# Kernel tuning notes

Measured on AMD Instinct MI355X. Metric: run time of the kernel, lower is better.

The kernel has to match this reference:

```python
import jax, jax.numpy as jnp
import numpy as np


def lstm(x, W, U, b):
    """Keras LSTM with activation='relu', recurrent_activation='sigmoid'.
    x: [B, S, E]; W: [E, 4u]; U: [u, 4u]; b: [4u]. Gate order i,f,c,o.
    Returns (all hidden states [B,S,u], last hidden [B,u])."""
    B = x.shape[0]
    u = U.shape[0]
    h0 = jnp.zeros((B, u), x.dtype)
    c0 = jnp.zeros((B, u), x.dtype)

    def step(carry, xt):
        h, c = carry
        z = xt @ W + h @ U + b
        i, f, g, o = jnp.split(z, 4, axis=-1)
        i = jax.nn.sigmoid(i)
        f = jax.nn.sigmoid(f)
        g = jax.nn.relu(g)          # candidate activation = relu
        o = jax.nn.sigmoid(o)
        c = f * c + i * g
        h = o * jax.nn.relu(c)      # output activation = relu
        return (h, c), h

    (hT, _), hs = jax.lax.scan(step, (h0, c0), jnp.swapaxes(x, 0, 1))
    return jnp.swapaxes(hs, 0, 1), hT


def setup_inputs() -> dict:
    key = jax.random.key(0)
    ks = iter(jax.random.split(key, 64))

    def W(*s):
        return jax.random.normal(next(ks), s, jnp.float32) * 0.05

    V = 32000
    inp = {
        "t": jax.random.randint(next(ks), (8, 16, 64), 0, V, jnp.int32),
        "p": jax.random.randint(next(ks), (8, 16, 512), 0, V, jnp.int32),
        "emb_t": W(V, 128),
        "emb_p": W(V, 256),
        # title LSTMs: 128 (return_seq) -> 64
        "tl0_W": W(128, 512), "tl0_U": W(128, 512), "tl0_b": jnp.zeros((512,), jnp.float32),
        "tl1_W": W(128, 256), "tl1_U": W(64, 256),  "tl1_b": jnp.zeros((256,), jnp.float32),
        # title dense: 128 relu, 64 relu, 32 linear
        "td0_W": W(64, 128),  "td0_b": jnp.zeros((128,), jnp.float32),
        "td1_W": W(128, 64),  "td1_b": jnp.zeros((64,), jnp.float32),
        "td2_W": W(64, 32),   "td2_b": jnp.zeros((32,), jnp.float32),
        # parag LSTMs: 256 (rs) -> 128 (rs) -> 64
        "pl0_W": W(256, 1024), "pl0_U": W(256, 1024), "pl0_b": jnp.zeros((1024,), jnp.float32),
        "pl1_W": W(256, 512),  "pl1_U": W(128, 512),  "pl1_b": jnp.zeros((512,), jnp.float32),
        "pl2_W": W(128, 256),  "pl2_U": W(64, 256),   "pl2_b": jnp.zeros((256,), jnp.float32),
        # parag dense: 128 relu, 64 relu, 32 linear
        "pd0_W": W(64, 128),  "pd0_b": jnp.zeros((128,), jnp.float32),
        "pd1_W": W(128, 64),  "pd1_b": jnp.zeros((64,), jnp.float32),
        "pd2_W": W(64, 32),   "pd2_b": jnp.zeros((32,), jnp.float32),
        # head: 256 relu, 128 relu, 64 relu, 32 sigmoid
        "L0_W": W(64, 256),  "L0_b": jnp.zeros((256,), jnp.float32),
        "L1_W": W(256, 128), "L1_b": jnp.zeros((128,), jnp.float32),
        "L2_W": W(128, 64),  "L2_b": jnp.zeros((64,), jnp.float32),
        "L3_W": W(64, 32),   "L3_b": jnp.zeros((32,), jnp.float32),
    }
    return inp


def reference(t, p, emb_t, emb_p,
              tl0_W, tl0_U, tl0_b, tl1_W, tl1_U, tl1_b,
              td0_W, td0_b, td1_W, td1_b, td2_W, td2_b,
              pl0_W, pl0_U, pl0_b, pl1_W, pl1_U, pl1_b, pl2_W, pl2_U, pl2_b,
              pd0_W, pd0_b, pd1_W, pd1_b, pd2_W, pd2_b,
              L0_W, L0_b, L1_W, L1_b, L2_W, L2_b, L3_W, L3_b):
    B, N, St = t.shape
    Sp = p.shape[2]

    # The original loops over B and map_fn over a singleton axis; the math is
    # identical to running the stacks on a flattened [B*N] recurrent batch.
    xt = emb_t[t.reshape(B * N, St)]              # [BN, St, 128]
    xt, _ = lstm(xt, tl0_W, tl0_U, tl0_b)         # [BN, St, 128]
    _, ht = lstm(xt, tl1_W, tl1_U, tl1_b)         # [BN, 64]
    ht = jax.nn.relu(ht @ td0_W + td0_b)
    ht = jax.nn.relu(ht @ td1_W + td1_b)
    ht = ht @ td2_W + td2_b                       # [BN, 32] (no activation)

    xp = emb_p[p.reshape(B * N, Sp)]              # [BN, Sp, 256]
    xp, _ = lstm(xp, pl0_W, pl0_U, pl0_b)
    xp, _ = lstm(xp, pl1_W, pl1_U, pl1_b)
    _, hp = lstm(xp, pl2_W, pl2_U, pl2_b)         # [BN, 64]
    hp = jax.nn.relu(hp @ pd0_W + pd0_b)
    hp = jax.nn.relu(hp @ pd1_W + pd1_b)
    hp = hp @ pd2_W + pd2_b                       # [BN, 32]

    feat = jnp.concatenate([ht, hp], axis=-1).reshape(B, N, 64)
    x = feat.mean(axis=1)                         # reduce_mean over axis=-2 (N)
    x = jax.nn.relu(x @ L0_W + L0_b)
    x = jax.nn.relu(x @ L1_W + L1_b)
    x = jax.nn.relu(x @ L2_W + L2_b)
    x = jax.nn.sigmoid(x @ L3_W + L3_b)           # [B, 32]
    return x
```

## Files before the change

kernel.cpp:

```cpp
#include <hip/hip_runtime.h>
#include <hip/hip_fp16.h>

typedef _Float16 f16;
typedef _Float16 f16x8 __attribute__((ext_vector_type(8)));
typedef float    f32x4 __attribute__((ext_vector_type(4)));
typedef unsigned short ushort;
typedef unsigned int uint;
typedef unsigned long long u64;

__device__ __forceinline__ float sigm(float x) { return 1.f / (1.f + __expf(-x)); }
__device__ __forceinline__ float reluf(float x) { return x > 0.f ? x : 0.f; }
__device__ __forceinline__ float h2f(ushort u) { return (float)__builtin_bit_cast(f16, u); }
__device__ __forceinline__ ushort f2h(float v) { return __builtin_bit_cast(ushort, (f16)v); }

#define LDRLX(p)    __hip_atomic_load((p), __ATOMIC_RELAXED, __HIP_MEMORY_SCOPE_AGENT)
#define STRLX(p, v) __hip_atomic_store((p), (v), __ATOMIC_RELAXED, __HIP_MEMORY_SCOPE_AGENT)
#define MFMA16(a, b, c) __builtin_amdgcn_mfma_f32_16x16x32_f16((a), (b), (c), 0, 0, 0)

__device__ __forceinline__ void poll_all(uint* p, uint need, bool act) {
  bool done = !act;
  while (true) {
    if (!done) done = (LDRLX(p) >= need);
    if (__all((int)done)) break;
    __builtin_amdgcn_s_sleep(1);
  }
}

__device__ __forceinline__ u64 ldr64(const u64* p) {
  return __hip_atomic_load(p, __ATOMIC_RELAXED, __HIP_MEMORY_SCOPE_AGENT);
}
__device__ __forceinline__ void str64(u64* p, u64 v) {
  __hip_atomic_store(p, v, __ATOMIC_RELAXED, __HIP_MEMORY_SCOPE_AGENT);
}

template <int NR>
__device__ __forceinline__ void poll_recs(const u64* const (&ra)[NR],
                                          const uint (&nd)[NR], u64 (&rv)[NR]) {
  bool ok[NR];
#pragma unroll
  for (int i = 0; i < NR; i++) ok[i] = (nd[i] == 0u);
  while (true) {
    bool all = true;
#pragma unroll
    for (int i = 0; i < NR; i++) if (!ok[i]) rv[i] = ldr64(ra[i]);
#pragma unroll
    for (int i = 0; i < NR; i++) if (!ok[i]) ok[i] = ((uint)(rv[i] >> 32) >= nd[i]);
#pragma unroll
    for (int i = 0; i < NR; i++) all &= ok[i];
    if (all) return;
    __builtin_amdgcn_s_sleep(1);
  }
}

template <int KF>
__global__ void pack_bsw(const float* __restrict__ B, f16* __restrict__ dst, int N) {
  int id = blockIdx.x * 256 + threadIdx.x;
  int total = KF * 32 * N;
  if (id >= total) return;
  int j  = id & 7;
  int L  = (id >> 3) & 63;
  int r  = id >> 9;
  int kf = r & (KF - 1);
  int c  = r / KF;
  int k  = kf * 32 + ((L >> 4) * 8) + j;
  int n  = c * 16 + (L & 15);
  dst[id] = (f16)B[k * N + n];
}

template <int Sx, int K, int KF, int N, int NC, int MODE>
__global__ __launch_bounds__(256) void gemm_xw(const int* __restrict__ tok,
                                               const float* __restrict__ emb,
                                               const f16* __restrict__ Bsw,
                                               const float* __restrict__ bias,
                                               f16* __restrict__ X) {
  __shared__ int tokLds[64];
  __shared__ f16x8 bLds[8 * 64];
  const int tid = threadIdx.x;
  const int blk = blockIdx.x;
  const int g  = (MODE == 0) ? (blk >> 7) : (blk >> 4);
  const int t0 = (MODE == 0) ? ((blk & 127) * 4) : ((blk & 15) * 4);
  if (tid < 64) {
    int wv = tid >> 4, rho = tid & 15;
    tokLds[tid] = tok[(g * 16 + rho) * Sx + t0 + wv];
  }
  __syncthreads();
  const int wave = tid >> 6, lane = tid & 63;
  const int quad = lane >> 4, l16 = lane & 15;

  f16x8 a[KF];
  {
    const float* arow = emb + (long)tokLds[wave * 16 + l16] * K + quad * 8;
#pragma unroll
    for (int kf = 0; kf < KF; kf++) {
      float4 v0 = *(const float4*)(arow + kf * 32);
      float4 v1 = *(const float4*)(arow + kf * 32 + 4);
      f16x8 tv;
      tv[0] = (f16)v0.x; tv[1] = (f16)v0.y; tv[2] = (f16)v0.z; tv[3] = (f16)v0.w;
      tv[4] = (f16)v1.x; tv[5] = (f16)v1.y; tv[6] = (f16)v1.z; tv[7] = (f16)v1.w;
      a[kf] = tv;
    }
  }
  const int t = t0 + wave;
  const f16x8* Bfrag = (const f16x8*)Bsw;
  for (int c = 0; c < NC; c++) {
    for (int i = tid; i < KF * 64; i += 256) bLds[i] = Bfrag[c * KF * 64 + i];
    __syncthreads();
    f32x4 acc = {0.f, 0.f, 0.f, 0.f};
#pragma unroll
    for (int kf = 0; kf < KF; kf++)
      acc = MFMA16(a[kf], bLds[kf * 64 + lane], acc);
    const int col = c * 16 + l16;
    const float bc = bias[col];
    uint2 pk;
    pk.x = (uint)f2h(acc[0] + bc) | ((uint)f2h(acc[1] + bc) << 16);
    pk.y = (uint)f2h(acc[2] + bc) | ((uint)f2h(acc[3] + bc) << 16);
    size_t base;
    if (MODE == 0) {
      int gm = col >> 8, u = col & 255;
      base = (((size_t)(g * 512 + t) * 4 + gm) * 4096) + u * 16 + quad * 4;
    } else {
      int gm = col >> 7, u = col & 127;
      base = (((size_t)(g * 64 + t) * 4 + gm) * 2048) + u * 16 + quad * 4;
    }
    *(uint2*)(X + base) = pk;
    __syncthreads();
  }
}

struct RP {
  const f16 *xp2, *xt2;
  const f16 *U0f, *W1f, *U1f, *W2f, *U2f, *U0tf, *W1tf, *U1tf;
  const float *pl1_b, *pl2_b, *tl1_b;
  const float *pd0W, *pd0b, *pd1W, *pd1b, *pd2W, *pd2b;
  const float *td0W, *td0b, *td1W, *td1b, *td2W, *td2b;
  u64 *h0r, *h1r, *h0tr;
  uint *cnt;
  float* feat;
};

__global__ __launch_bounds__(256, 1) void recur_pipe(RP A) {
  __shared__ __align__(16) char smem[147968];
  const int tid = threadIdx.x;
  const int w = tid >> 6, lane = tid & 63;
  const int quad = lane >> 4, l16 = lane & 15;
  const int blk = blockIdx.x;
  const int role = blk >> 3, g = blk & 7;
  uint* mytag = A.cnt + (role * 8 + g) * 16;

  if (role < 4) {
    const int bb = role;
    f16* wlds = (f16*)smem;
    f16* hb   = (f16*)(smem + 131072);
    {
      const uint4* U0q = (const uint4*)A.U0f;
      uint4* wq = (uint4*)wlds;
      for (int idx = tid; idx < 8192; idx += 256) {
        int gm = idx >> 11, r = idx & 2047, wv = r >> 9, kf = (r >> 6) & 7, ln = r & 63;
        wq[idx] = U0q[((gm * 16 + 4 * bb + wv) * 8 + kf) * 64 + ln];
      }
    }
    for (int idx = tid; idx < 4224; idx += 256) hb[idx] = (f16)0.f;
    float c0[4] = {0.f, 0.f, 0.f, 0.f};
    u64* ringg = A.h0r + (size_t)g * 16384;
    int pp[3]; { int q = 0; for (int p = 0; p < 4; p++) if (p != bb) pp[q++] = p; }
    const uint2* xq2 = (const uint2*)A.xp2;
    const f16x8* wv8 = (const f16x8*)wlds;
    const int myu = 64 * bb + 16 * w + l16;
    uint* bpp = A.cnt;
    if (lane < 4) bpp = A.cnt + ((4 + lane) * 8 + g) * 16;
    __syncthreads();

    for (int t = 0; t < 512; t++) {
      uint2 xv[4];
      {
        size_t xb = ((size_t)(g * 512 + t) * 4) * 1024 + (size_t)myu * 4 + quad;
#pragma unroll
        for (int gm = 0; gm < 4; gm++) xv[gm] = xq2[xb + (size_t)gm * 1024];
      }
      {
        bool act = (lane < 4) && (t > 0) && ((t & 3) == 0);
        uint need = t > 4 ? (uint)(t - 4) : 0u;
        poll_all(bpp, need, act);
      }
      {
        const u64* slotb = ringg + (size_t)((t + 7) & 7) * 2048;
        const u64* ra[6]; uint nd[6]; u64 rv[6];
#pragma unroll
        for (int q = 0; q < 3; q++) {
          const u64* rb = slotb + pp[q] * 512 + 2 * tid;
          ra[q * 2] = rb; ra[q * 2 + 1] = rb + 1;
          nd[q * 2] = nd[q * 2 + 1] = (t > 0) ? (uint)t : 0u;
        }
        poll_recs<6>(ra, nd, rv);
        if (t > 0) {
          f16* dst = hb + (t & 1) * 4224;
          const int ul = tid >> 2;
#pragma unroll
          for (int q = 0; q < 3; q++)
#pragma unroll
            for (int j = 0; j < 2; j++) {
              uint pay = (uint)rv[q * 2 + j];
              int r0 = ((tid & 3) * 2 + j) * 2;
              dst[r0 * 264 + pp[q] * 64 + ul] = __builtin_bit_cast(f16, (ushort)pay);
              dst[(r0 + 1) * 264 + pp[q] * 64 + ul] = __builtin_bit_cast(f16, (ushort)(pay >> 16));
            }
        }
      }
      __syncthreads();
      f16x8 af[8];
#pragma unroll
      for (int kf = 0; kf < 8; kf++)
        af[kf] = *(const f16x8*)&hb[(t & 1) * 4224 + l16 * 264 + kf * 32 + quad * 8];
      f32x4 z[4];
#pragma unroll
      for (int gm = 0; gm < 4; gm++) {
        f32x4 zz = {0.f, 0.f, 0.f, 0.f};
#pragma unroll
        for (int kf = 0; kf < 8; kf++)
          zz = MFMA16(af[kf], wv8[((gm * 4 + w) * 8 + kf) * 64 + lane], zz);
        z[gm] = zz;
      }
      u64 xs[4];
#pragma unroll
      for (int gm = 0; gm < 4; gm++) xs[gm] = ((u64)xv[gm].y << 32) | xv[gm].x;
      ushort hs[4];
      f16* wbuf = hb + ((t + 1) & 1) * 4224;
#pragma unroll
      for (int r = 0; r < 4; r++) {
        float gi = sigm(z[0][r] + h2f((ushort)(xs[0] >> (16 * r))));
        float ff = sigm(z[1][r] + h2f((ushort)(xs[1] >> (16 * r))));
        float gg = reluf(z[2][r] + h2f((ushort)(xs[2] >> (16 * r))));
        float oo = sigm(z[3][r] + h2f((ushort)(xs[3] >> (16 * r))));
        c0[r] = ff * c0[r] + gi * gg;
        hs[r] = f2h(oo * reluf(c0[r]));
        wbuf[(quad * 4 + r) * 264 + myu] = __builtin_bit_cast(f16, hs[r]);
      }
      {
        u64 tg = ((u64)(uint)(t + 1)) << 32;
        u64* wb = ringg + (size_t)(t & 7) * 2048 + bb * 512 + (16 * w + l16) * 8 + quad * 2;
        str64(wb,     tg | (u64)((uint)hs[0] | ((uint)hs[1] << 16)));
        str64(wb + 1, tg | (u64)((uint)hs[2] | ((uint)hs[3] << 16)));
      }
    }
  } else if (role < 8) {
    const int bn = role - 4;
    f16* wlds = (f16*)smem;
    f16* h0c  = (f16*)(smem + 98304);
    f16* h1b  = (f16*)(smem + 106752);
    float* zL = (float*)(smem + 115456);
    {
      const uint4* W1q = (const uint4*)A.W1f;
      const uint4* U1q = (const uint4*)A.U1f;
      uint4* wq = (uint4*)wlds;
      for (int idx = tid; idx < 4096; idx += 256) {
        int gm = idx >> 10, r = idx & 1023, j2 = r >> 9, kf = (r >> 6) & 7, ln = r & 63;
        wq[idx] = W1q[((gm * 8 + bn * 2 + j2) * 8 + kf) * 64 + ln];
      }
      for (int idx = tid; idx < 2048; idx += 256) {
        int gm = idx >> 9, r = idx & 511, j2 = r >> 8, kf = (r >> 6) & 3, ln = r & 63;
        wq[4096 + idx] = U1q[((gm * 8 + bn * 2 + j2) * 4 + kf) * 64 + ln];
      }
    }
    for (int idx = tid; idx < 2176; idx += 256) h1b[idx] = (f16)0.f;
    float c1[2] = {0.f, 0.f};
    float bth[4];
    { int un = tid & 31; for (int gm = 0; gm < 4; gm++) bth[gm] = A.pl1_b[gm * 128 + 32 * bn + un]; }
    u64* h0rg = A.h0r + (size_t)g * 16384;
    u64* h1rg = A.h1r + (size_t)g * 8192;
    int pp[3]; { int q = 0; for (int p = 0; p < 4; p++) if (p != bn) pp[q++] = p; }
    const f16x8* wv8 = (const f16x8*)wlds;
    uint* bpp = A.cnt + (8 * 8 + g) * 16;
    __syncthreads();

    for (int t = 0; t < 512; t++) {
      {
        bool act = (lane == 0) && ((t & 3) == 0);
        uint need = t > 4 ? (uint)(t - 4) : 0u;
        poll_all(bpp, need, act);
      }
      const u64* ra[11]; uint nd[11]; u64 rv[11];
      {
        const u64* s0b = h0rg + (size_t)(t & 7) * 2048;
#pragma unroll
        for (int e = 0; e < 8; e++) { ra[e] = s0b + tid + 256 * e; nd[e] = (uint)(t + 1); }
        const u64* s1b = h1rg + (size_t)((t + 7) & 7) * 1024;
#pragma unroll
        for (int q = 0; q < 3; q++) { ra[8 + q] = s1b + pp[q] * 256 + tid; nd[8 + q] = (t > 0) ? (uint)t : 0u; }
      }
      poll_recs<11>(ra, nd, rv);
      {
#pragma unroll
        for (int e = 0; e < 8; e++) {
          int idx = tid + 256 * e;
          int q = idx >> 9, rr = idx & 511, uls = rr >> 3, rp = rr & 7;
          uint pay = (uint)rv[e];
          h0c[(2 * rp) * 264 + q * 64 + uls]     = __builtin_bit_cast(f16, (ushort)pay);
          h0c[(2 * rp + 1) * 264 + q * 64 + uls] = __builtin_bit_cast(f16, (ushort)(pay >> 16));
        }
        if (t > 0) {
          f16* dst = h1b + (t & 1) * 2176;
          int un = tid >> 3, sq = tid & 7;
#pragma unroll
          for (int q = 0; q < 3; q++) {
            uint pay = (uint)rv[8 + q];
            dst[sq * 136 + pp[q] * 32 + un]       = __builtin_bit_cast(f16, (ushort)pay);
            dst[(sq + 8) * 136 + pp[q] * 32 + un] = __builtin_bit_cast(f16, (ushort)(pay >> 16));
          }
        }
      }
      __syncthreads();
      if (tid == 0) STRLX(mytag, (uint)(t + 1));
      f16x8 af0[8], af1[4];
#pragma unroll
      for (int kf = 0; kf < 8; kf++)
        af0[kf] = *(const f16x8*)&h0c[l16 * 264 + kf * 32 + quad * 8];
#pragma unroll
      for (int kf = 0; kf < 4; kf++)
        af1[kf] = *(const f16x8*)&h1b[(t & 1) * 2176 + l16 * 136 + kf * 32 + quad * 8];
#pragma unroll
      for (int j2 = 0; j2 < 2; j2++) {
        f32x4 zz = {0.f, 0.f, 0.f, 0.f};
#pragma unroll
        for (int kf = 0; kf < 8; kf++)
          zz = MFMA16(af0[kf], wv8[((w * 2 + j2) * 8 + kf) * 64 + lane], zz);
#pragma unroll
        for (int kf = 0; kf < 4; kf++)
          zz = MFMA16(af1[kf], wv8[4096 + ((w * 2 + j2) * 4 + kf) * 64 + lane], zz);
#pragma unroll
        for (int r = 0; r < 4; r++)
          zL[(quad * 4 + r) * 132 + w * 32 + j2 * 16 + l16] = zz[r];
      }
      __syncthreads();
      {
        int sq = tid >> 5, un = tid & 31;
        f16* dst = h1b + ((t + 1) & 1) * 2176;
        ushort hh[2];
#pragma unroll
        for (int e = 0; e < 2; e++) {
          int s = sq + 8 * e;
          float gi = sigm(zL[s * 132 + un] + bth[0]);
          float ff = sigm(zL[s * 132 + 32 + un] + bth[1]);
          float gg = reluf(zL[s * 132 + 64 + un] + bth[2]);
          float oo = sigm(zL[s * 132 + 96 + un] + bth[3]);
          c1[e] = ff * c1[e] + gi * gg;
          float hv = oo * reluf(c1[e]);
          hh[e] = f2h(hv);
          dst[s * 136 + 32 * bn + un] = __builtin_bit_cast(f16, hh[e]);
        }
        u64 tg = ((u64)(uint)(t + 1)) << 32;
        str64(h1rg + (size_t)(t & 7) * 1024 + bn * 256 + un * 8 + sq,
              tg | (u64)((uint)hh[0] | ((uint)hh[1] << 16)));
      }
    }
  } else if (role == 8) {
    f16* wlds = (f16*)smem;
    f16* h1c  = (f16*)(smem + 98304);
    f16* h2db = (f16*)(smem + 107008);
    {
      const uint4* W2q = (const uint4*)A.W2f;
      const uint4* U2q = (const uint4*)A.U2f;
      uint4* wq = (uint4*)wlds;
      for (int idx = tid; idx < 4096; idx += 256) wq[idx] = W2q[idx];
      for (int idx = tid; idx < 2048; idx += 256) wq[4096 + idx] = U2q[idx];
    }
    for (int idx = tid; idx < 1152; idx += 256) h2db[idx] = (f16)0.f;
    float c2[4] = {0.f, 0.f, 0.f, 0.f};
    float b2[4];
#pragma unroll
    for (int gm = 0; gm < 4; gm++) b2[gm] = A.pl2_b[gm * 64 + 16 * w + l16];
    u64* h1rg = A.h1r + (size_t)g * 8192;
    const f16x8* wv8 = (const f16x8*)wlds;
    __syncthreads();

    for (int t = 0; t < 512; t++) {
      const u64* ra[4]; uint nd[4]; u64 rv[4];
      {
        const u64* s1b = h1rg + (size_t)(t & 7) * 1024;
#pragma unroll
        for (int e = 0; e < 4; e++) { ra[e] = s1b + tid + 256 * e; nd[e] = (uint)(t + 1); }
      }
      poll_recs<4>(ra, nd, rv);
      {
        f16* dst = h1c + (t & 1) * 2176;
#pragma unroll
        for (int e = 0; e < 4; e++) {
          int idx = tid + 256 * e;
          int bq = idx >> 8, rr = idx & 255, un = rr >> 3, sq = rr & 7;
          uint pay = (uint)rv[e];
          dst[sq * 136 + bq * 32 + un]       = __builtin_bit_cast(f16, (ushort)pay);
          dst[(sq + 8) * 136 + bq * 32 + un] = __builtin_bit_cast(f16, (ushort)(pay >> 16));
        }
      }
      __syncthreads();
      if (tid == 0) STRLX(mytag, (uint)(t + 1));
      f16x8 af0[4], af1[2];
#pragma unroll
      for (int kf = 0; kf < 4; kf++)
        af0[kf] = *(const f16x8*)&h1c[(t & 1) * 2176 + l16 * 136 + kf * 32 + quad * 8];
#pragma unroll
      for (int kf = 0; kf < 2; kf++)
        af1[kf] = *(const f16x8*)&h2db[(t & 1) * 1152 + l16 * 72 + kf * 32 + quad * 8];
      f32x4 z[4];
#pragma unroll
      for (int gm = 0; gm < 4; gm++) {
        f32x4 zz = {0.f, 0.f, 0.f, 0.f};
#pragma unroll
        for (int kf = 0; kf < 4; kf++)
          zz = MFMA16(af0[kf], wv8[((gm * 4 + w) * 4 + kf) * 64 + lane], zz);
#pragma unroll
        for (int kf = 0; kf < 2; kf++)
          zz = MFMA16(af1[kf], wv8[4096 + ((gm * 4 + w) * 2 + kf) * 64 + lane], zz);
        z[gm] = zz;
      }
#pragma unroll
      for (int r = 0; r < 4; r++) {
        float gi = sigm(z[0][r] + b2[0]);
        float ff = sigm(z[1][r] + b2[1]);
        float gg = reluf(z[2][r] + b2[2]);
        float oo = sigm(z[3][r] + b2[3]);
        c2[r] = ff * c2[r] + gi * gg;
        h2db[((t + 1) & 1) * 1152 + (quad * 4 + r) * 72 + 16 * w + l16] = (f16)(oo * reluf(c2[r]));
      }
    }
    __syncthreads();
    float* zmA = (float*)smem;
    float* zmB = (float*)(smem + 8448);
    const f16* hf = h2db;
#pragma unroll 1
    for (int e = 0; e < 8; e++) {
      const int idx = tid + 256 * e, sq = idx >> 7, j = idx & 127;
      float a = A.pd0b[j];
      for (int k = 0; k < 64; k++) a += (float)hf[sq * 72 + k] * A.pd0W[k * 128 + j];
      zmA[sq * 132 + j] = reluf(a);
    }
    __syncthreads();
#pragma unroll 1
    for (int e = 0; e < 4; e++) {
      const int idx = tid + 256 * e, sq = idx >> 6, j = idx & 63;
      float a = A.pd1b[j];
      for (int k = 0; k < 128; k++) a += zmA[sq * 132 + k] * A.pd1W[k * 64 + j];
      zmB[sq * 68 + j] = reluf(a);
    }
    __syncthreads();
#pragma unroll 1
    for (int e = 0; e < 2; e++) {
      const int idx = tid + 256 * e, sq = idx >> 5, j = idx & 31;
      float a = A.pd2b[j];
      for (int k = 0; k < 64; k++) a += zmB[sq * 68 + k] * A.pd2W[k * 32 + j];
      A.feat[(g * 16 + sq) * 64 + 32 + j] = a;
    }
  } else if (role < 11) {
    const int bb = role - 9;
    f16* wlds = (f16*)smem;
    f16* hb   = (f16*)(smem + 65536);
    {
      const uint4* U0tq = (const uint4*)A.U0tf;
      uint4* wq = (uint4*)wlds;
      for (int idx = tid; idx < 4096; idx += 256) {
        int gm = idx >> 10, r = idx & 1023, wv = r >> 8, kf = (r >> 6) & 3, ln = r & 63;
        wq[idx] = U0tq[((gm * 8 + 4 * bb + wv) * 4 + kf) * 64 + ln];
      }
    }
    for (int idx = tid; idx < 2176; idx += 256) hb[idx] = (f16)0.f;
    float c0[4] = {0.f, 0.f, 0.f, 0.f};
    u64* ringg = A.h0tr + (size_t)g * 8192;
    const uint2* xq2 = (const uint2*)A.xt2;
    const f16x8* wv8 = (const f16x8*)wlds;
    const int myu = 64 * bb + 16 * w + l16;
    const int pbb = bb ^ 1;
    uint* bpp = A.cnt + (11 * 8 + g) * 16;
    __syncthreads();

    for (int t = 0; t < 64; t++) {
      uint2 xv[4];
      {
        size_t xb = ((size_t)(g * 64 + t) * 4) * 512 + (size_t)myu * 4 + quad;
#pragma unroll
        for (int gm = 0; gm < 4; gm++) xv[gm] = xq2[xb + (size_t)gm * 512];
      }
      {
        bool act = (lane == 0) && (t > 0) && ((t & 3) == 0);
        uint need = t > 4 ? (uint)(t - 4) : 0u;
        poll_all(bpp, need, act);
      }
      {
        const u64* ra[2]; uint nd[2]; u64 rv[2];
        const u64* rb = ringg + (size_t)((t + 7) & 7) * 1024 + pbb * 512 + 2 * tid;
        ra[0] = rb; ra[1] = rb + 1;
        nd[0] = nd[1] = (t > 0) ? (uint)t : 0u;
        poll_recs<2>(ra, nd, rv);
        if (t > 0) {
          f16* dst = hb + (t & 1) * 2176;
          const int ul = tid >> 2;
#pragma unroll
          for (int j = 0; j < 2; j++) {
            uint pay = (uint)rv[j];
            int r0 = ((tid & 3) * 2 + j) * 2;
            dst[r0 * 136 + pbb * 64 + ul]       = __builtin_bit_cast(f16, (ushort)pay);
            dst[(r0 + 1) * 136 + pbb * 64 + ul] = __builtin_bit_cast(f16, (ushort)(pay >> 16));
          }
        }
      }
      __syncthreads();
      f16x8 af[4];
#pragma unroll
      for (int kf = 0; kf < 4; kf++)
        af[kf] = *(const f16x8*)&hb[(t & 1) * 2176 + l16 * 136 + kf * 32 + quad * 8];
      f32x4 z[4];
#pragma unroll
      for (int gm = 0; gm < 4; gm++) {
        f32x4 zz = {0.f, 0.f, 0.f, 0.f};
#pragma unroll
        for (int kf = 0; kf < 4; kf++)
          zz = MFMA16(af[kf], wv8[((gm * 4 + w) * 4 + kf) * 64 + lane], zz);
        z[gm] = zz;
      }
      u64 xs[4];
#pragma unroll
      for (int gm = 0; gm < 4; gm++) xs[gm] = ((u64)xv[gm].y << 32) | xv[gm].x;
      ushort hs[4];
      f16* wbuf = hb + ((t + 1) & 1) * 2176;
#pragma unroll
      for (int r = 0; r < 4; r++) {
        float gi = sigm(z[0][r] + h2f((ushort)(xs[0] >> (16 * r))));
        float ff = sigm(z[1][r] + h2f((ushort)(xs[1] >> (16 * r))));
        float gg = reluf(z[2][r] + h2f((ushort)(xs[2] >> (16 * r))));
        float oo = sigm(z[3][r] + h2f((ushort)(xs[3] >> (16 * r))));
        c0[r] = ff * c0[r] + gi * gg;
        hs[r] = f2h(oo * reluf(c0[r]));
        wbuf[(quad * 4 + r) * 136 + myu] = __builtin_bit_cast(f16, hs[r]);
      }
      {
        u64 tg = ((u64)(uint)(t + 1)) << 32;
        u64* wb = ringg + (size_t)(t & 7) * 1024 + bb * 512 + (16 * w + l16) * 8 + quad * 2;
        str64(wb,     tg | (u64)((uint)hs[0] | ((uint)hs[1] << 16)));
        str64(wb + 1, tg | (u64)((uint)hs[2] | ((uint)hs[3] << 16)));
      }
    }
  } else {
    f16* wlds = (f16*)smem;
    f16* h0tc = (f16*)(smem + 98304);
    f16* h1db = (f16*)(smem + 107008);
    {
      const uint4* W1tq = (const uint4*)A.W1tf;
      const uint4* U1tq = (const uint4*)A.U1tf;
      uint4* wq = (uint4*)wlds;
      for (int idx = tid; idx < 4096; idx += 256) wq[idx] = W1tq[idx];
      for (int idx = tid; idx < 2048; idx += 256) wq[4096 + idx] = U1tq[idx];
    }
    for (int idx = tid; idx < 1152; idx += 256) h1db[idx] = (f16)0.f;
    float c1[4] = {0.f, 0.f, 0.f, 0.f};
    float bt[4];
#pragma unroll
    for (int gm = 0; gm < 4; gm++) bt[gm] = A.tl1_b[gm * 64 + 16 * w + l16];
    u64* ringg = A.h0tr + (size_t)g * 8192;
    const f16x8* wv8 = (const f16x8*)wlds;
    __syncthreads();

    for (int t = 0; t < 64; t++) {
      const u64* ra[4]; uint nd[4]; u64 rv[4];
      {
        const u64* base = ringg + (size_t)(t & 7) * 1024;
#pragma unroll
        for (int e = 0; e < 4; e++) { ra[e] = base + tid + 256 * e; nd[e] = (uint)(t + 1); }
      }
      poll_recs<4>(ra, nd, rv);
      {
        f16* dst = h0tc + (t & 1) * 2176;
#pragma unroll
        for (int e = 0; e < 4; e++) {
          int idx = tid + 256 * e;
          int q = idx >> 9, rr = idx & 511, uls = rr >> 3, rp = rr & 7;
          uint pay = (uint)rv[e];
          dst[(2 * rp) * 136 + q * 64 + uls]     = __builtin_bit_cast(f16, (ushort)pay);
          dst[(2 * rp + 1) * 136 + q * 64 + uls] = __builtin_bit_cast(f16, (ushort)(pay >> 16));
        }
      }
      __syncthreads();
      if (tid == 0) STRLX(mytag, (uint)(t + 1));
      f16x8 af0[4], af1[2];
#pragma unroll
      for (int kf = 0; kf < 4; kf++)
        af0[kf] = *(const f16x8*)&h0tc[(t & 1) * 2176 + l16 * 136 + kf * 32 + quad * 8];
#pragma unroll
      for (int kf = 0; kf < 2; kf++)
        af1[kf] = *(const f16x8*)&h1db[(t & 1) * 1152 + l16 * 72 + kf * 32 + quad * 8];
      f32x4 z[4];
#pragma unroll
      for (int gm = 0; gm < 4; gm++) {
        f32x4 zz = {0.f, 0.f, 0.f, 0.f};
#pragma unroll
        for (int kf = 0; kf < 4; kf++)
          zz = MFMA16(af0[kf], wv8[((gm * 4 + w) * 4 + kf) * 64 + lane], zz);
#pragma unroll
        for (int kf = 0; kf < 2; kf++)
          zz = MFMA16(af1[kf], wv8[4096 + ((gm * 4 + w) * 2 + kf) * 64 + lane], zz);
        z[gm] = zz;
      }
#pragma unroll
      for (int r = 0; r < 4; r++) {
        float gi = sigm(z[0][r] + bt[0]);
        float ff = sigm(z[1][r] + bt[1]);
        float gg = reluf(z[2][r] + bt[2]);
        float oo = sigm(z[3][r] + bt[3]);
        c1[r] = ff * c1[r] + gi * gg;
        h1db[((t + 1) & 1) * 1152 + (quad * 4 + r) * 72 + 16 * w + l16] = (f16)(oo * reluf(c1[r]));
      }
    }
    __syncthreads();
    float* zmA = (float*)smem;
    float* zmB = (float*)(smem + 8448);
    const f16* hf = h1db;
#pragma unroll 1
    for (int e = 0; e < 8; e++) {
      const int idx = tid + 256 * e, sq = idx >> 7, j = idx & 127;
      float a = A.td0b[j];
      for (int k = 0; k < 64; k++) a += (float)hf[sq * 72 + k] * A.td0W[k * 128 + j];
      zmA[sq * 132 + j] = reluf(a);
    }
    __syncthreads();
#pragma unroll 1
    for (int e = 0; e < 4; e++) {
      const int idx = tid + 256 * e, sq = idx >> 6, j = idx & 63;
      float a = A.td1b[j];
      for (int k = 0; k < 128; k++) a += zmA[sq * 132 + k] * A.td1W[k * 64 + j];
      zmB[sq * 68 + j] = reluf(a);
    }
    __syncthreads();
#pragma unroll 1
    for (int e = 0; e < 2; e++) {
      const int idx = tid + 256 * e, sq = idx >> 5, j = idx & 31;
      float a = A.td2b[j];
      for (int k = 0; k < 64; k++) a += zmB[sq * 68 + k] * A.td2W[k * 32 + j];
      A.feat[(g * 16 + sq) * 64 + j] = a;
    }
  }
}

__global__ __launch_bounds__(256) void head_kernel(const float* __restrict__ feat,
    const float* __restrict__ L0W, const float* __restrict__ L0b,
    const float* __restrict__ L1W, const float* __restrict__ L1b,
    const float* __restrict__ L2W, const float* __restrict__ L2b,
    const float* __restrict__ L3W, const float* __restrict__ L3b,
    float* __restrict__ out) {
  __shared__ float xb[512];
  __shared__ float y0[2048];
  __shared__ float y1[1024];
  __shared__ float y2[512];
  const int tid = threadIdx.x;
  for (int idx = tid; idx < 512; idx += 256) {
    int b = idx >> 6, d = idx & 63;
    float s = 0.f;
    for (int n = 0; n < 16; n++) s += feat[(b * 16 + n) * 64 + d];
    xb[idx] = s * (1.f / 16.f);
  }
  __syncthreads();
  for (int idx = tid; idx < 2048; idx += 256) {
    int b = idx >> 8, j = idx & 255;
    float a = L0b[j];
    for (int k = 0; k < 64; k++) a += xb[b * 64 + k] * L0W[k * 256 + j];
    y0[idx] = reluf(a);
  }
  __syncthreads();
  for (int idx = tid; idx < 1024; idx += 256) {
    int b = idx >> 7, j = idx & 127;
    float a = L1b[j];
    for (int k = 0; k < 256; k++) a += y0[b * 256 + k] * L1W[k * 128 + j];
    y1[idx] = reluf(a);
  }
  __syncthreads();
  for (int idx = tid; idx < 512; idx += 256) {
    int b = idx >> 6, j = idx & 63;
    float a = L2b[j];
    for (int k = 0; k < 128; k++) a += y1[b * 128 + k] * L2W[k * 64 + j];
    y2[idx] = reluf(a);
  }
  __syncthreads();
  {
    int b = tid >> 5, j = tid & 31;
    float a = L3b[j];
    for (int k = 0; k < 64; k++) a += y2[b * 64 + k] * L3W[k * 32 + j];
    out[b * 32 + j] = 1.f / (1.f + __expf(-a));
  }
}

extern "C" void kernel_launch(void* const* d_in, const int* in_sizes, int n_in,
                              void* d_out, int out_size, void* d_ws, size_t ws_size,
                              hipStream_t stream) {
  const int*   t_tok = (const int*)d_in[0];
  const int*   p_tok = (const int*)d_in[1];
  const float* emb_t = (const float*)d_in[2];
  const float* emb_p = (const float*)d_in[3];
  const float* tl0_W = (const float*)d_in[4];
  const float* tl0_U = (const float*)d_in[5];
  const float* tl0_b = (const float*)d_in[6];
  const float* tl1_W = (const float*)d_in[7];
  const float* tl1_U = (const float*)d_in[8];
  const float* tl1_b = (const float*)d_in[9];
  const float* td0_W = (const float*)d_in[10];
  const float* td0_b = (const float*)d_in[11];
  const float* td1_W = (const float*)d_in[12];
  const float* td1_b = (const float*)d_in[13];
  const float* td2_W = (const float*)d_in[14];
  const float* td2_b = (const float*)d_in[15];
  const float* pl0_W = (const float*)d_in[16];
  const float* pl0_U = (const float*)d_in[17];
  const float* pl0_b = (const float*)d_in[18];
  const float* pl1_W = (const float*)d_in[19];
  const float* pl1_U = (const float*)d_in[20];
  const float* pl1_b = (const float*)d_in[21];
  const float* pl2_W = (const float*)d_in[22];
  const float* pl2_U = (const float*)d_in[23];
  const float* pl2_b = (const float*)d_in[24];
  const float* pd0_W = (const float*)d_in[25];
  const float* pd0_b = (const float*)d_in[26];
  const float* pd1_W = (const float*)d_in[27];
  const float* pd1_b = (const float*)d_in[28];
  const float* pd2_W = (const float*)d_in[29];
  const float* pd2_b = (const float*)d_in[30];
  const float* L0_W  = (const float*)d_in[31];
  const float* L0_b  = (const float*)d_in[32];
  const float* L1_W  = (const float*)d_in[33];
  const float* L1_b  = (const float*)d_in[34];
  const float* L2_W  = (const float*)d_in[35];
  const float* L2_b  = (const float*)d_in[36];
  const float* L3_W  = (const float*)d_in[37];
  const float* L3_b  = (const float*)d_in[38];

  char* ws = (char*)d_ws;
  size_t off = 0;
  auto alloc = [&](size_t bytes) {
    void* ptr = ws + off;
    off += (bytes + 255) & ~(size_t)255;
    return ptr;
  };
  f16* xp2  = (f16*)alloc((size_t)8 * 512 * 4 * 4096 * 2);
  f16* xt2  = (f16*)alloc((size_t)8 * 64 * 4 * 2048 * 2);
  f16* Bp   = (f16*)alloc((size_t)256 * 1024 * 2);
  f16* Bt   = (f16*)alloc((size_t)128 * 512 * 2);
  f16* U0f  = (f16*)alloc((size_t)256 * 1024 * 2);
  f16* W1f  = (f16*)alloc((size_t)256 * 512 * 2);
  f16* U1f  = (f16*)alloc((size_t)128 * 512 * 2);
  f16* W2f  = (f16*)alloc((size_t)128 * 256 * 2);
  f16* U2f  = (f16*)alloc((size_t)64 * 256 * 2);
  f16* U0tf = (f16*)alloc((size_t)128 * 512 * 2);
  f16* W1tf = (f16*)alloc((size_t)128 * 256 * 2);
  f16* U1tf = (f16*)alloc((size_t)64 * 256 * 2);
  size_t ringoff = off;
  u64* h0r  = (u64*)alloc((size_t)8 * 16384 * 8);
  u64* h1r  = (u64*)alloc((size_t)8 * 8192 * 8);
  u64* h0tr = (u64*)alloc((size_t)8 * 8192 * 8);
  uint* cnt = (uint*)alloc((size_t)96 * 16 * 4);
  size_t ringlen = off - ringoff;
  float* feat = (float*)alloc((size_t)128 * 64 * 4);

  hipMemsetAsync(ws + ringoff, 0, ringlen, stream);

  pack_bsw<8><<<1024, 256, 0, stream>>>(pl0_W, Bp, 1024);
  pack_bsw<4><<<256, 256, 0, stream>>>(tl0_W, Bt, 512);
  pack_bsw<8><<<1024, 256, 0, stream>>>(pl0_U, U0f, 1024);
  pack_bsw<8><<<512, 256, 0, stream>>>(pl1_W, W1f, 512);
  pack_bsw<4><<<256, 256, 0, stream>>>(pl1_U, U1f, 512);
  pack_bsw<4><<<128, 256, 0, stream>>>(pl2_W, W2f, 256);
  pack_bsw<2><<<64, 256, 0, stream>>>(pl2_U, U2f, 256);
  pack_bsw<4><<<256, 256, 0, stream>>>(tl0_U, U0tf, 512);
  pack_bsw<4><<<128, 256, 0, stream>>>(tl1_W, W1tf, 256);
  pack_bsw<2><<<64, 256, 0, stream>>>(tl1_U, U1tf, 256);
  gemm_xw<512, 256, 8, 1024, 64, 0><<<1024, 256, 0, stream>>>(p_tok, emb_p, Bp, pl0_b, xp2);
  gemm_xw<64, 128, 4, 512, 32, 1><<<128, 256, 0, stream>>>(t_tok, emb_t, Bt, tl0_b, xt2);

  RP ra;
  ra.xp2 = xp2; ra.xt2 = xt2;
  ra.U0f = U0f; ra.W1f = W1f; ra.U1f = U1f; ra.W2f = W2f; ra.U2f = U2f;
  ra.U0tf = U0tf; ra.W1tf = W1tf; ra.U1tf = U1tf;
  ra.pl1_b = pl1_b; ra.pl2_b = pl2_b; ra.tl1_b = tl1_b;
  ra.pd0W = pd0_W; ra.pd0b = pd0_b; ra.pd1W = pd1_W; ra.pd1b = pd1_b;
  ra.pd2W = pd2_W; ra.pd2b = pd2_b;
  ra.td0W = td0_W; ra.td0b = td0_b; ra.td1W = td1_W; ra.td1b = td1_b;
  ra.td2W = td2_W; ra.td2b = td2_b;
  ra.h0r = h0r; ra.h1r = h1r; ra.h0tr = h0tr; ra.cnt = cnt;
  ra.feat = feat;
  recur_pipe<<<96, 256, 0, stream>>>(ra);

  head_kernel<<<1, 256, 0, stream>>>(feat, L0_W, L0_b, L1_W, L1_b, L2_W, L2_b,
                                     L3_W, L3_b, (float*)d_out);
}
```

Measured before the change: 1.508 ms.

## Merge per-layer split blocks into single 1024-thread blocks with register-resident weights

Each LSTM layer previously spread across four 256-thread blocks that exchanged hidden-state slices through global ring buffers every timestep. Now each layer and group runs in one 1024-thread block, so recurrent state is shared via LDS and __syncthreads instead of cross-block polling. Weights are held in VGPRs instead of LDS, and the grid shrinks from 96 to 40 blocks. This targets the per-step inter-block synchronization latency. In exchange, register pressure rises at 1024 threads, some waves sit idle in the smaller layers, and fewer CUs share the work.

Result: slower. 4.582 ms (+203.9%).

```diff
diff --git a/kernel.cpp b/kernel.cpp
--- a/kernel.cpp
+++ b/kernel.cpp
@@ -138,36 +138,33 @@
   float* feat;
 };
 
-__global__ __launch_bounds__(256, 1) void recur_pipe(RP A) {
-  __shared__ __align__(16) char smem[147968];
+__global__ __launch_bounds__(1024, 1) void recur_pipe(RP A) {
+  __shared__ __align__(16) char smem[21504];
   const int tid = threadIdx.x;
-  const int w = tid >> 6, lane = tid & 63;
+  const int w16 = tid >> 6, lane = tid & 63;
   const int quad = lane >> 4, l16 = lane & 15;
   const int blk = blockIdx.x;
   const int role = blk >> 3, g = blk & 7;
   uint* mytag = A.cnt + (role * 8 + g) * 16;
 
-  if (role < 4) {
-    const int bb = role;
-    f16* wlds = (f16*)smem;
-    f16* hb   = (f16*)(smem + 131072);
+  if (role == 0) {
+    const int bb = w16 >> 2, w = w16 & 3;
+    f16* hb = (f16*)smem;
+    f16x8 wr[4][8];
     {
-      const uint4* U0q = (const uint4*)A.U0f;
-      uint4* wq = (uint4*)wlds;
-      for (int idx = tid; idx < 8192; idx += 256) {
-        int gm = idx >> 11, r = idx & 2047, wv = r >> 9, kf = (r >> 6) & 7, ln = r & 63;
-        wq[idx] = U0q[((gm * 16 + 4 * bb + wv) * 8 + kf) * 64 + ln];
-      }
-    }
-    for (int idx = tid; idx < 4224; idx += 256) hb[idx] = (f16)0.f;
+      const f16x8* U0f8 = (const f16x8*)A.U0f;
+#pragma unroll
+      for (int gm = 0; gm < 4; gm++)
+#pragma unroll
+        for (int kf = 0; kf < 8; kf++)
+          wr[gm][kf] = U0f8[((gm * 16 + 4 * bb + w) * 8 + kf) * 64 + lane];
+    }
+    for (int idx = tid; idx < 8448; idx += 1024) hb[idx] = (f16)0.f;
     float c0[4] = {0.f, 0.f, 0.f, 0.f};
     u64* ringg = A.h0r + (size_t)g * 16384;
-    int pp[3]; { int q = 0; for (int p = 0; p < 4; p++) if (p != bb) pp[q++] = p; }
     const uint2* xq2 = (const uint2*)A.xp2;
-    const f16x8* wv8 = (const f16x8*)wlds;
     const int myu = 64 * bb + 16 * w + l16;
-    uint* bpp = A.cnt;
-    if (lane < 4) bpp = A.cnt + ((4 + lane) * 8 + g) * 16;
+    uint* bpp = A.cnt + (1 * 8 + g) * 16;
     __syncthreads();
 
     for (int t = 0; t < 512; t++) {
@@ -177,36 +174,8 @@
 #pragma unroll
         for (int gm = 0; gm < 4; gm++) xv[gm] = xq2[xb + (size_t)gm * 1024];
       }
-      {
-        bool act = (lane < 4) && (t > 0) && ((t & 3) == 0);
-        uint need = t > 4 ? (uint)(t - 4) : 0u;
-        poll_all(bpp, need, act);
-      }
-      {
-        const u64* slotb = ringg + (size_t)((t + 7) & 7) * 2048;
-        const u64* ra[6]; uint nd[6]; u64 rv[6];
-#pragma unroll
-        for (int q = 0; q < 3; q++) {
-          const u64* rb = slotb + pp[q] * 512 + 2 * tid;
-          ra[q * 2] = rb; ra[q * 2 + 1] = rb + 1;
-          nd[q * 2] = nd[q * 2 + 1] = (t > 0) ? (uint)t : 0u;
-        }
-        poll_recs<6>(ra, nd, rv);
-        if (t > 0) {
-          f16* dst = hb + (t & 1) * 4224;
-          const int ul = tid >> 2;
-#pragma unroll
-          for (int q = 0; q < 3; q++)
-#pragma unroll
-            for (int j = 0; j < 2; j++) {
-              uint pay = (uint)rv[q * 2 + j];
-              int r0 = ((tid & 3) * 2 + j) * 2;
-              dst[r0 * 264 + pp[q] * 64 + ul] = __builtin_bit_cast(f16, (ushort)pay);
-              dst[(r0 + 1) * 264 + pp[q] * 64 + ul] = __builtin_bit_cast(f16, (ushort)(pay >> 16));
-            }
-        }
-      }
-      __syncthreads();
+      poll_all(bpp, t > 4 ? (uint)(t - 4) : 0u,
+               (lane == 0) && (t > 0) && ((t & 3) == 0));
       f16x8 af[8];
 #pragma unroll
       for (int kf = 0; kf < 8; kf++)
@@ -217,7 +186,7 @@
         f32x4 zz = {0.f, 0.f, 0.f, 0.f};
 #pragma unroll
         for (int kf = 0; kf < 8; kf++)
-          zz = MFMA16(af[kf], wv8[((gm * 4 + w) * 8 + kf) * 64 + lane], zz);
+          zz = MFMA16(af[kf], wr[gm][kf], zz);
         z[gm] = zz;
       }
       u64 xs[4];
@@ -235,6 +204,7 @@
         hs[r] = f2h(oo * reluf(c0[r]));
         wbuf[(quad * 4 + r) * 264 + myu] = __builtin_bit_cast(f16, hs[r]);
       }
+      __syncthreads();
       {
         u64 tg = ((u64)(uint)(t + 1)) << 32;
         u64* wb = ringg + (size_t)(t & 7) * 2048 + bb * 512 + (16 * w + l16) * 8 + quad * 2;
@@ -242,295 +212,254 @@
         str64(wb + 1, tg | (u64)((uint)hs[2] | ((uint)hs[3] << 16)));
       }
     }
-  } else if (role < 8) {
-    const int bn = role - 4;
-    f16* wlds = (f16*)smem;
-    f16* h0c  = (f16*)(smem + 98304);
-    f16* h1b  = (f16*)(smem + 106752);
-    float* zL = (float*)(smem + 115456);
-    {
-      const uint4* W1q = (const uint4*)A.W1f;
-      const uint4* U1q = (const uint4*)A.U1f;
-      uint4* wq = (uint4*)wlds;
-      for (int idx = tid; idx < 4096; idx += 256) {
-        int gm = idx >> 10, r = idx & 1023, j2 = r >> 9, kf = (r >> 6) & 7, ln = r & 63;
-        wq[idx] = W1q[((gm * 8 + bn * 2 + j2) * 8 + kf) * 64 + ln];
-      }
-      for (int idx = tid; idx < 2048; idx += 256) {
-        int gm = idx >> 9, r = idx & 511, j2 = r >> 8, kf = (r >> 6) & 3, ln = r & 63;
-        wq[4096 + idx] = U1q[((gm * 8 + bn * 2 + j2) * 4 + kf) * 64 + ln];
-      }
-    }
-    for (int idx = tid; idx < 2176; idx += 256) h1b[idx] = (f16)0.f;
-    float c1[2] = {0.f, 0.f};
+  } else if (role == 1) {
+    f16* h0c = (f16*)smem;
+    f16* h1b = (f16*)(smem + 8448);
+    f16x8 wrA[4][8], wrB[4][4];
+    if (w16 < 8) {
+      const f16x8* W1f8 = (const f16x8*)A.W1f;
+      const f16x8* U1f8 = (const f16x8*)A.U1f;
+#pragma unroll
+      for (int gm = 0; gm < 4; gm++) {
+#pragma unroll
+        for (int kf = 0; kf < 8; kf++)
+          wrA[gm][kf] = W1f8[((gm * 8 + w16) * 8 + kf) * 64 + lane];
+#pragma unroll
+        for (int kf = 0; kf < 4; kf++)
+          wrB[gm][kf] = U1f8[((gm * 8 + w16) * 4 + kf) * 64 + lane];
+      }
+    }
+    for (int idx = tid; idx < 4352; idx += 1024) h1b[idx] = (f16)0.f;
+    float c1[4] = {0.f, 0.f, 0.f, 0.f};
+    const int un = 16 * w16 + l16;
     float bth[4];
-    { int un = tid & 31; for (int gm = 0; gm < 4; gm++) bth[gm] = A.pl1_b[gm * 128 + 32 * bn + un]; }
+    if (w16 < 8) {
+#pragma unroll
+      for (int gm = 0; gm < 4; gm++) bth[gm] = A.pl1_b[gm * 128 + un];
+    }
     u64* h0rg = A.h0r + (size_t)g * 16384;
     u64* h1rg = A.h1r + (size_t)g * 8192;
-    int pp[3]; { int q = 0; for (int p = 0; p < 4; p++) if (p != bn) pp[q++] = p; }
-    const f16x8* wv8 = (const f16x8*)wlds;
-    uint* bpp = A.cnt + (8 * 8 + g) * 16;
+    uint* bpp = A.cnt + (2 * 8 + g) * 16;
     __syncthreads();
 
     for (int t = 0; t < 512; t++) {
-      {
-        bool act = (lane == 0) && ((t & 3) == 0);
-        uint need = t > 4 ? (uint)(t - 4) : 0u;
-        poll_all(bpp, need, act);
-      }
-      const u64* ra[11]; uint nd[11]; u64 rv[11];
+      poll_all(bpp, t > 4 ? (uint)(t - 4) : 0u, (lane == 0) && ((t & 3) == 0));
+      const u64* ra[2]; uint nd[2]; u64 rv[2];
       {
         const u64* s0b = h0rg + (size_t)(t & 7) * 2048;
-#pragma unroll
-        for (int e = 0; e < 8; e++) { ra[e] = s0b + tid + 256 * e; nd[e] = (uint)(t + 1); }
-        const u64* s1b = h1rg + (size_t)((t + 7) & 7) * 1024;
-#pragma unroll
-        for (int q = 0; q < 3; q++) { ra[8 + q] = s1b + pp[q] * 256 + tid; nd[8 + q] = (t > 0) ? (uint)t : 0u; }
-      }
-      poll_recs<11>(ra, nd, rv);
-      {
-#pragma unroll
-        for (int e = 0; e < 8; e++) {
-          int idx = tid + 256 * e;
-          int q = idx >> 9, rr = idx & 511, uls = rr >> 3, rp = rr & 7;
-          uint pay = (uint)rv[e];
-          h0c[(2 * rp) * 264 + q * 64 + uls]     = __builtin_bit_cast(f16, (ushort)pay);
-          h0c[(2 * rp + 1) * 264 + q * 64 + uls] = __builtin_bit_cast(f16, (ushort)(pay >> 16));
-        }
-        if (t > 0) {
-          f16* dst = h1b + (t & 1) * 2176;
-          int un = tid >> 3, sq = tid & 7;
-#pragma unroll
-          for (int q = 0; q < 3; q++) {
-            uint pay = (uint)rv[8 + q];
-            dst[sq * 136 + pp[q] * 32 + un]       = __builtin_bit_cast(f16, (ushort)pay);
-            dst[(sq + 8) * 136 + pp[q] * 32 + un] = __builtin_bit_cast(f16, (ushort)(pay >> 16));
-          }
-        }
+        ra[0] = s0b + tid; ra[1] = s0b + tid + 1024;
+        nd[0] = nd[1] = (uint)(t + 1);
+      }
+      poll_recs<2>(ra, nd, rv);
+#pragma unroll
+      for (int e = 0; e < 2; e++) {
+        int idx = tid + 1024 * e;
+        int q = idx >> 9, rr = idx & 511, uls = rr >> 3, rp = rr & 7;
+        uint pay = (uint)rv[e];
+        h0c[(2 * rp) * 264 + q * 64 + uls]     = __builtin_bit_cast(f16, (ushort)pay);
+        h0c[(2 * rp + 1) * 264 + q * 64 + uls] = __builtin_bit_cast(f16, (ushort)(pay >> 16));
       }
       __syncthreads();
       if (tid == 0) STRLX(mytag, (uint)(t + 1));
-      f16x8 af0[8], af1[4];
-#pragma unroll
-      for (int kf = 0; kf < 8; kf++)
-        af0[kf] = *(const f16x8*)&h0c[l16 * 264 + kf * 32 + quad * 8];
-#pragma unroll
-      for (int kf = 0; kf < 4; kf++)
-        af1[kf] = *(const f16x8*)&h1b[(t & 1) * 2176 + l16 * 136 + kf * 32 + quad * 8];
-#pragma unroll
-      for (int j2 = 0; j2 < 2; j2++) {
-        f32x4 zz = {0.f, 0.f, 0.f, 0.f};
+      ushort hs[4];
+      if (w16 < 8) {
+        f16x8 af0[8], af1[4];
 #pragma unroll
         for (int kf = 0; kf < 8; kf++)
-          zz = MFMA16(af0[kf], wv8[((w * 2 + j2) * 8 + kf) * 64 + lane], zz);
+          af0[kf] = *(const f16x8*)&h0c[l16 * 264 + kf * 32 + quad * 8];
 #pragma unroll
         for (int kf = 0; kf < 4; kf++)
-          zz = MFMA16(af1[kf], wv8[4096 + ((w * 2 + j2) * 4 + kf) * 64 + lane], zz);
-#pragma unroll
-        for (int r = 0; r < 4; r++)
-          zL[(quad * 4 + r) * 132 + w * 32 + j2 * 16 + l16] = zz[r];
+          af1[kf] = *(const f16x8*)&h1b[(t & 1) * 2176 + l16 * 136 + kf * 32 + quad * 8];
+        f32x4 z[4];
+#pragma unroll
+        for (int gm = 0; gm < 4; gm++) {
+          f32x4 zz = {0.f, 0.f, 0.f, 0.f};
+#pragma unroll
+          for (int kf = 0; kf < 8; kf++)
+            zz = MFMA16(af0[kf], wrA[gm][kf], zz);
+#pragma unroll
+          for (int kf = 0; kf < 4; kf++)
+            zz = MFMA16(af1[kf], wrB[gm][kf], zz);
+          z[gm] = zz;
+        }
+        f16* dst = h1b + ((t + 1) & 1) * 2176;
+#pragma unroll
+        for (int r = 0; r < 4; r++) {
+          float gi = sigm(z[0][r] + bth[0]);
+          float ff = sigm(z[1][r] + bth[1]);
+          float gg = reluf(z[2][r] + bth[2]);
+          float oo = sigm(z[3][r] + bth[3]);
+          c1[r] = ff * c1[r] + gi * gg;
+          hs[r] = f2h(oo * reluf(c1[r]));
+          dst[(quad * 4 + r) * 136 + un] = __builtin_bit_cast(f16, hs[r]);
+        }
       }
       __syncthreads();
-      {
-        int sq = tid >> 5, un = tid & 31;
-        f16* dst = h1b + ((t + 1) & 1) * 2176;
-        ushort hh[2];
-#pragma unroll
-        for (int e = 0; e < 2; e++) {
-          int s = sq + 8 * e;
-          float gi = sigm(zL[s * 132 + un] + bth[0]);
-          float ff = sigm(zL[s * 132 + 32 + un] + bth[1]);
-          float gg = reluf(zL[s * 132 + 64 + un] + bth[2]);
-          float oo = sigm(zL[s * 132 + 96 + un] + bth[3]);
-          c1[e] = ff * c1[e] + gi * gg;
-          float hv = oo * reluf(c1[e]);
-          hh[e] = f2h(hv);
-          dst[s * 136 + 32 * bn + un] = __builtin_bit_cast(f16, hh[e]);
-        }
+      if (w16 < 8) {
         u64 tg = ((u64)(uint)(t + 1)) << 32;
-        str64(h1rg + (size_t)(t & 7) * 1024 + bn * 256 + un * 8 + sq,
-              tg | (u64)((uint)hh[0] | ((uint)hh[1] << 16)));
-      }
-    }
-  } else if (role == 8) {
-    f16* wlds = (f16*)smem;
-    f16* h1c  = (f16*)(smem + 98304);
-    f16* h2db = (f16*)(smem + 107008);
-    {
-      const uint4* W2q = (const uint4*)A.W2f;
-      const uint4* U2q = (const uint4*)A.U2f;
-      uint4* wq = (uint4*)wlds;
-      for (int idx = tid; idx < 4096; idx += 256) wq[idx] = W2q[idx];
-      for (int idx = tid; idx < 2048; idx += 256) wq[4096 + idx] = U2q[idx];
-    }
-    for (int idx = tid; idx < 1152; idx += 256) h2db[idx] = (f16)0.f;
+        u64* wb = h1rg + (size_t)(t & 7) * 1024 + un * 8 + quad * 2;
+        str64(wb,     tg | (u64)((uint)hs[0] | ((uint)hs[1] << 16)));
+        str64(wb + 1, tg | (u64)((uint)hs[2] | ((uint)hs[3] << 16)));
+      }
+    }
+  } else if (role == 2) {
+    f16* h1c  = (f16*)smem;
+    f16* h2db = (f16*)(smem + 16384);
+    f16x8 wrA[4][4], wrB[4][2];
+    if (tid < 256) {
+      const f16x8* W2f8 = (const f16x8*)A.W2f;
+      const f16x8* U2f8 = (const f16x8*)A.U2f;
+#pragma unroll
+      for (int gm = 0; gm < 4; gm++) {
+#pragma unroll
+        for (int kf = 0; kf < 4; kf++)
+          wrA[gm][kf] = W2f8[((gm * 4 + w16) * 4 + kf) * 64 + lane];
+#pragma unroll
+        for (int kf = 0; kf < 2; kf++)
+          wrB[gm][kf] = U2f8[((gm * 4 + w16) * 2 + kf) * 64 + lane];
+      }
+    }
+    for (int idx = tid; idx < 2304; idx += 1024) h2db[idx] = (f16)0.f;
     float c2[4] = {0.f, 0.f, 0.f, 0.f};
     float b2[4];
-#pragma unroll
-    for (int gm = 0; gm < 4; gm++) b2[gm] = A.pl2_b[gm * 64 + 16 * w + l16];
+    if (tid < 256) {
+#pragma unroll
+      for (int gm = 0; gm < 4; gm++) b2[gm] = A.pl2_b[gm * 64 + 16 * w16 + l16];
+    }
     u64* h1rg = A.h1r + (size_t)g * 8192;
-    const f16x8* wv8 = (const f16x8*)wlds;
     __syncthreads();
 
     for (int t = 0; t < 512; t++) {
-      const u64* ra[4]; uint nd[4]; u64 rv[4];
+      const u64* ra[1]; uint nd[1]; u64 rv[1];
+      ra[0] = h1rg + (size_t)(t & 7) * 1024 + tid;
+      nd[0] = (uint)(t + 1);
+      poll_recs<1>(ra, nd, rv);
       {
-        const u64* s1b = h1rg + (size_t)(t & 7) * 1024;
-#pragma unroll
-        for (int e = 0; e < 4; e++) { ra[e] = s1b + tid + 256 * e; nd[e] = (uint)(t + 1); }
-      }
-      poll_recs<4>(ra, nd, rv);
-      {
-        f16* dst = h1c + (t & 1) * 2176;
-#pragma unroll
-        for (int e = 0; e < 4; e++) {
-          int idx = tid + 256 * e;
-          int bq = idx >> 8, rr = idx & 255, un = rr >> 3, sq = rr & 7;
-          uint pay = (uint)rv[e];
-          dst[sq * 136 + bq * 32 + un]       = __builtin_bit_cast(f16, (ushort)pay);
-          dst[(sq + 8) * 136 + bq * 32 + un] = __builtin_bit_cast(f16, (ushort)(pay >> 16));
-        }
+        int un = tid >> 3, rp = tid & 7;
+        uint pay = (uint)rv[0];
+        h1c[(2 * rp) * 136 + un]     = __builtin_bit_cast(f16, (ushort)pay);
+        h1c[(2 * rp + 1) * 136 + un] = __builtin_bit_cast(f16, (ushort)(pay >> 16));
       }
       __syncthreads();
       if (tid == 0) STRLX(mytag, (uint)(t + 1));
-      f16x8 af0[4], af1[2];
-#pragma unroll
-      for (int kf = 0; kf < 4; kf++)
-        af0[kf] = *(const f16x8*)&h1c[(t & 1) * 2176 + l16 * 136 + kf * 32 + quad * 8];
-#pragma unroll
-      for (int kf = 0; kf < 2; kf++)
-        af1[kf] = *(const f16x8*)&h2db[(t & 1) * 1152 + l16 * 72 + kf * 32 + quad * 8];
-      f32x4 z[4];
-#pragma unroll
-      for (int gm = 0; gm < 4; gm++) {
-        f32x4 zz = {0.f, 0.f, 0.f, 0.f};
+      if (tid < 256) {
+        f16x8 af0[4], af1[2];
 #pragma unroll
         for (int kf = 0; kf < 4; kf++)
-          zz = MFMA16(af0[kf], wv8[((gm * 4 + w) * 4 + kf) * 64 + lane], zz);
+          af0[kf] = *(const f16x8*)&h1c[l16 * 136 + kf * 32 + quad * 8];
 #pragma unroll
         for (int kf = 0; kf < 2; kf++)
-          zz = MFMA16(af1[kf], wv8[4096 + ((gm * 4 + w) * 2 + kf) * 64 + lane], zz);
-        z[gm] = zz;
-      }
-#pragma unroll
-      for (int r = 0; r < 4; r++) {
-        float gi = sigm(z[0][r] + b2[0]);
-        float ff = sigm(z[1][r] + b2[1]);
-        float gg = reluf(z[2][r] + b2[2]);
-        float oo = sigm(z[3][r] + b2[3]);
-        c2[r] = ff * c2[r] + gi * gg;
-        h2db[((t + 1) & 1) * 1152 + (quad * 4 + r) * 72 + 16 * w + l16] = (f16)(oo * reluf(c2[r]));
-      }
-    }
-    __syncthreads();
+          af1[kf] = *(const f16x8*)&h2db[(t & 1) * 1152 + l16 * 72 + kf * 32 + quad * 8];
+        f32x4 z[4];
+#pragma unroll
+        for (int gm = 0; gm < 4; gm++) {
+          f32x4 zz = {0.f, 0.f, 0.f, 0.f};
+#pragma unroll
+          for (int kf = 0; kf < 4; kf++)
+            zz = MFMA16(af0[kf], wrA[gm][kf], zz);
+#pragma unroll
+          for (int kf = 0; kf < 2; kf++)
+            zz = MFMA16(af1[kf], wrB[gm][kf], zz);
+          z[gm] = zz;
+        }
+#pragma unroll
+        for (int r = 0; r < 4; r++) {
+          float gi = sigm(z[0][r] + b2[0]);
+          float ff = sigm(z[1][r] + b2[1]);
+          float gg = reluf(z[2][r] + b2[2]);
+          float oo = sigm(z[3][r] + b2[3]);
+          c2[r] = ff * c2[r] + gi * gg;
+          h2db[((t + 1) & 1) * 1152 + (quad * 4 + r) * 72 + 16 * w16 + l16] =
+              (f16)(oo * reluf(c2[r]));
+        }
+      }
+      __syncthreads();
+    }
     float* zmA = (float*)smem;
     float* zmB = (float*)(smem + 8448);
     const f16* hf = h2db;
 #pragma unroll 1
-    for (int e = 0; e < 8; e++) {
-      const int idx = tid + 256 * e, sq = idx >> 7, j = idx & 127;
+    for (int e = 0; e < 2; e++) {
+      const int idx = tid + 1024 * e, sq = idx >> 7, j = idx & 127;
       float a = A.pd0b[j];
       for (int k = 0; k < 64; k++) a += (float)hf[sq * 72 + k] * A.pd0W[k * 128 + j];
       zmA[sq * 132 + j] = reluf(a);
     }
     __syncthreads();
-#pragma unroll 1
-    for (int e = 0; e < 4; e++) {
-      const int idx = tid + 256 * e, sq = idx >> 6, j = idx & 63;
+    {
+      const int sq = tid >> 6, j = tid & 63;
       float a = A.pd1b[j];
       for (int k = 0; k < 128; k++) a += zmA[sq * 132 + k] * A.pd1W[k * 64 + j];
       zmB[sq * 68 + j] = reluf(a);
     }
     __syncthreads();
-#pragma unroll 1
-    for (int e = 0; e < 2; e++) {
-      const int idx = tid + 256 * e, sq = idx >> 5, j = idx & 31;
+    if (tid < 512) {
+      const int sq = tid >> 5, j = tid & 31;
       float a = A.pd2b[j];
       for (int k = 0; k < 64; k++) a += zmB[sq * 68 + k] * A.pd2W[k * 32 + j];
       A.feat[(g * 16 + sq) * 64 + 32 + j] = a;
     }
-  } else if (role < 11) {
-    const int bb = role - 9;
-    f16* wlds = (f16*)smem;
-    f16* hb   = (f16*)(smem + 65536);
-    {
-      const uint4* U0tq = (const uint4*)A.U0tf;
-      uint4* wq = (uint4*)wlds;
-      for (int idx = tid; idx < 4096; idx += 256) {
-        int gm = idx >> 10, r = idx & 1023, wv = r >> 8, kf = (r >> 6) & 3, ln = r & 63;
-        wq[idx] = U0tq[((gm * 8 + 4 * bb + wv) * 4 + kf) * 64 + ln];
-      }
-    }
-    for (int idx = tid; idx < 2176; idx += 256) hb[idx] = (f16)0.f;
+  } else if (role == 3) {
+    const int bb = w16 >> 2, w = w16 & 3;
+    f16* hb = (f16*)smem;
+    f16x8 wr[4][4];
+    if (w16 < 8) {
+      const f16x8* U0tf8 = (const f16x8*)A.U0tf;
+#pragma unroll
+      for (int gm = 0; gm < 4; gm++)
+#pragma unroll
+        for (int kf = 0; kf < 4; kf++)
+          wr[gm][kf] = U0tf8[((gm * 8 + 4 * bb + w) * 4 + kf) * 64 + lane];
+    }
+    for (int idx = tid; idx < 4352; idx += 1024) hb[idx] = (f16)0.f;
     float c0[4] = {0.f, 0.f, 0.f, 0.f};
     u64* ringg = A.h0tr + (size_t)g * 8192;
     const uint2* xq2 = (const uint2*)A.xt2;
-    const f16x8* wv8 = (const f16x8*)wlds;
     const int myu = 64 * bb + 16 * w + l16;
-    const int pbb = bb ^ 1;
-    uint* bpp = A.cnt + (11 * 8 + g) * 16;
+    uint* bpp = A.cnt + (4 * 8 + g) * 16;
     __syncthreads();
 
     for (int t = 0; t < 64; t++) {
-      uint2 xv[4];
-      {
-        size_t xb = ((size_t)(g * 64 + t) * 4) * 512 + (size_t)myu * 4 + quad;
-#pragma unroll
-        for (int gm = 0; gm < 4; gm++) xv[gm] = xq2[xb + (size_t)gm * 512];
-      }
-      {
-        bool act = (lane == 0) && (t > 0) && ((t & 3) == 0);
-        uint need = t > 4 ? (uint)(t - 4) : 0u;
-        poll_all(bpp, need, act);
-      }
-      {
-        const u64* ra[2]; uint nd[2]; u64 rv[2];
-        const u64* rb = ringg + (size_t)((t + 7) & 7) * 1024 + pbb * 512 + 2 * tid;
-        ra[0] = rb; ra[1] = rb + 1;
-        nd[0] = nd[1] = (t > 0) ? (uint)t : 0u;
-        poll_recs<2>(ra, nd, rv);
-        if (t > 0) {
-          f16* dst = hb + (t & 1) * 2176;
-          const int ul = tid >> 2;
-#pragma unroll
-          for (int j = 0; j < 2; j++) {
-            uint pay = (uint)rv[j];
-            int r0 = ((tid & 3) * 2 + j) * 2;
-            dst[r0 * 136 + pbb * 64 + ul]       = __builtin_bit_cast(f16, (ushort)pay);
-            dst[(r0 + 1) * 136 + pbb * 64 + ul] = __builtin_bit_cast(f16, (ushort)(pay >> 16));
-          }
+      ushort hs[4];
+      if (w16 < 8) {
+        uint2 xv[4];
+        {
+          size_t xb = ((size_t)(g * 64 + t) * 4) * 512 + (size_t)myu * 4 + quad;
+#pragma unroll
+          for (int gm = 0; gm < 4; gm++) xv[gm] = xq2[xb + (size_t)gm * 512];
+        }
+        poll_all(bpp, t > 4 ? (uint)(t - 4) : 0u,
+                 (lane == 0) && (t > 0) && ((t & 3) == 0));
+        f16x8 af[4];
+#pragma unroll
+        for (int kf = 0; kf < 4; kf++)
+          af[kf] = *(const f16x8*)&hb[(t & 1) * 2176 + l16 * 136 + kf * 32 + quad * 8];
+        f32x4 z[4];
+#pragma unroll
+        for (int gm = 0; gm < 4; gm++) {
+          f32x4 zz = {0.f, 0.f, 0.f, 0.f};
+#pragma unroll
+          for (int kf = 0; kf < 4; kf++)
+            zz = MFMA16(af[kf], wr[gm][kf], zz);
+          z[gm] = zz;
+        }
+        u64 xs[4];
+#pragma unroll
+        for (int gm = 0; gm < 4; gm++) xs[gm] = ((u64)xv[gm].y << 32) | xv[gm].x;
+        f16* wbuf = hb + ((t + 1) & 1) * 2176;
+#pragma unroll
+        for (int r = 0; r < 4; r++) {
+          float gi = sigm(z[0][r] + h2f((ushort)(xs[0] >> (16 * r))));
+          float ff = sigm(z[1][r] + h2f((ushort)(xs[1] >> (16 * r))));
+          float gg = reluf(z[2][r] + h2f((ushort)(xs[2] >> (16 * r))));
+          float oo = sigm(z[3][r] + h2f((ushort)(xs[3] >> (16 * r))));
+          c0[r] = ff * c0[r] + gi * gg;
+          hs[r] = f2h(oo * reluf(c0[r]));
+          wbuf[(quad * 4 + r) * 136 + myu] = __builtin_bit_cast(f16, hs[r]);
         }
       }
       __syncthreads();
-      f16x8 af[4];
-#pragma unroll
-      for (int kf = 0; kf < 4; kf++)
-        af[kf] = *(const f16x8*)&hb[(t & 1) * 2176 + l16 * 136 + kf * 32 + quad * 8];
-      f32x4 z[4];
-#pragma unroll
-      for (int gm = 0; gm < 4; gm++) {
-        f32x4 zz = {0.f, 0.f, 0.f, 0.f};
-#pragma unroll
-        for (int kf = 0; kf < 4; kf++)
-          zz = MFMA16(af[kf], wv8[((gm * 4 + w) * 4 + kf) * 64 + lane], zz);
-        z[gm] = zz;
-      }
-      u64 xs[4];
-#pragma unroll
-      for (int gm = 0; gm < 4; gm++) xs[gm] = ((u64)xv[gm].y << 32) | xv[gm].x;
-      ushort hs[4];
-      f16* wbuf = hb + ((t + 1) & 1) * 2176;
-#pragma unroll
-      for (int r = 0; r < 4; r++) {
-        float gi = sigm(z[0][r] + h2f((ushort)(xs[0] >> (16 * r))));
-        float ff = sigm(z[1][r] + h2f((ushort)(xs[1] >> (16 * r))));
-        float gg = reluf(z[2][r] + h2f((ushort)(xs[2] >> (16 * r))));
-        float oo = sigm(z[3][r] + h2f((ushort)(xs[3] >> (16 * r))));
-        c0[r] = ff * c0[r] + gi * gg;
-        hs[r] = f2h(oo * reluf(c0[r]));
-        wbuf[(quad * 4 + r) * 136 + myu] = __builtin_bit_cast(f16, hs[r]);
-      }
-      {
+      if (w16 < 8) {
         u64 tg = ((u64)(uint)(t + 1)) << 32;
         u64* wb = ringg + (size_t)(t & 7) * 1024 + bb * 512 + (16 * w + l16) * 8 + quad * 2;
         str64(wb,     tg | (u64)((uint)hs[0] | ((uint)hs[1] << 16)));
@@ -538,73 +467,76 @@
       }
     }
   } else {
-    f16* wlds = (f16*)smem;
-    f16* h0tc = (f16*)(smem + 98304);
-    f16* h1db = (f16*)(smem + 107008);
-    {
-      const uint4* W1tq = (const uint4*)A.W1tf;
-      const uint4* U1tq = (const uint4*)A.U1tf;
-      uint4* wq = (uint4*)wlds;
-      for (int idx = tid; idx < 4096; idx += 256) wq[idx] = W1tq[idx];
-      for (int idx = tid; idx < 2048; idx += 256) wq[4096 + idx] = U1tq[idx];
-    }
-    for (int idx = tid; idx < 1152; idx += 256) h1db[idx] = (f16)0.f;
+    f16* h0tc = (f16*)smem;
+    f16* h1db = (f16*)(smem + 16384);
+    f16x8 wrA[4][4], wrB[4][2];
+    if (tid < 256) {
+      const f16x8* W1tf8 = (const f16x8*)A.W1tf;
+      const f16x8* U1tf8 = (const f16x8*)A.U1tf;
+#pragma unroll
+      for (int gm = 0; gm < 4; gm++) {
+#pragma unroll
+        for (int kf = 0; kf < 4; kf++)
+          wrA[gm][kf] = W1tf8[((gm * 4 + w16) * 4 + kf) * 64 + lane];
+#pragma unroll
+        for (int kf = 0; kf < 2; kf++)
+          wrB[gm][kf] = U1tf8[((gm * 4 + w16) * 2 + kf) * 64 + lane];
+      }
+    }
+    for (int idx = tid; idx < 2304; idx += 1024) h1db[idx] = (f16)0.f;
     float c1[4] = {0.f, 0.f, 0.f, 0.f};
     float bt[4];
-#pragma unroll
-    for (int gm = 0; gm < 4; gm++) bt[gm] = A.tl1_b[gm * 64 + 16 * w + l16];
+    if (tid < 256) {
+#pragma unroll
+      for (int gm = 0; gm < 4; gm++) bt[gm] = A.tl1_b[gm * 64 + 16 * w16 + l16];
+    }
     u64* ringg = A.h0tr + (size_t)g * 8192;
-    const f16x8* wv8 = (const f16x8*)wlds;
     __syncthreads();
 
     for (int t = 0; t < 64; t++) {
-      const u64* ra[4]; uint nd[4]; u64 rv[4];
-      {
-        const u64* base = ringg + (size_t)(t & 7) * 1024;
-#pragma unroll
-        for (int e = 0; e < 4; e++) { ra[e] = base + tid + 256 * e; nd[e] = (uint)(t + 1); }
-      }
-      poll_recs<4>(ra, nd, rv);
+      const u64* ra[1]; uint nd[1]; u64 rv[1];
+      ra[0] = ringg + (size_t)(t & 7) * 1024 + tid;
+      nd[0] = (uint)(t + 1);
+      poll_recs<1>(ra, nd, rv);
       {
         f16* dst = h0tc + (t & 1) * 2176;
-#pragma unroll
-        for (int e = 0; e < 4; e++) {
-          int idx = tid + 256 * e;
-          int q = idx >> 9, rr = idx & 511, uls = rr >> 3, rp = rr & 7;
-          uint pay = (uint)rv[e];
-          dst[(2 * rp) * 136 + q * 64 + uls]     = __builtin_bit_cast(f16, (ushort)pay);
-          dst[(2 * rp + 1) * 136 + q * 64 + uls] = __builtin_bit_cast(f16, (ushort)(pay >> 16));
-        }
+        int q = tid >> 9, rr = tid & 511, uls = rr >> 3, rp = rr & 7;
+        uint pay = (uint)rv[0];
+        dst[(2 * rp) * 136 + q * 64 + uls]     = __builtin_bit_cast(f16, (ushort)pay);
+        dst[(2 * rp + 1) * 136 + q * 64 + uls] = __builtin_bit_cast(f16, (ushort)(pay >> 16));
       }
       __syncthreads();
       if (tid == 0) STRLX(mytag, (uint)(t + 1));
-      f16x8 af0[4], af1[2];
-#pragma unroll
-      for (int kf = 0; kf < 4; kf++)
-        af0[kf] = *(const f16x8*)&h0tc[(t & 1) * 2176 + l16 * 136 + kf * 32 + quad * 8];
-#pragma unroll
-      for (int kf = 0; kf < 2; kf++)
-        af1[kf] = *(const f16x8*)&h1db[(t & 1) * 1152 + l16 * 72 + kf * 32 + quad * 8];
-      f32x4 z[4];
-#pragma unroll
-      for (int gm = 0; gm < 4; gm++) {
-        f32x4 zz = {0.f, 0.f, 0.f, 0.f};
+      if (tid < 256) {
+        f16x8 af0[4], af1[2];
 #pragma unroll
         for (int kf = 0; kf < 4; kf++)
-          zz = MFMA16(af0[kf], wv8[((gm * 4 + w) * 4 + kf) * 64 + lane], zz);
+          af0[kf] = *(const f16x8*)&h0tc[(t & 1) * 2176 + l16 * 136 + kf * 32 + quad * 8];
 #pragma unroll
         for (int kf = 0; kf < 2; kf++)
-          zz = MFMA16(af1[kf], wv8[4096 + ((gm * 4 + w) * 2 + kf) * 64 + lane], zz);
-        z[gm] = zz;
-      }
-#pragma unroll
-      for (int r = 0; r < 4; r++) {
-        float gi = sigm(z[0][r] + bt[0]);
-        float ff = sigm(z[1][r] + bt[1]);
-        float gg = reluf(z[2][r] + bt[2]);
-        float oo = sigm(z[3][r] + bt[3]);
-        c1[r] = ff * c1[r] + gi * gg;
-        h1db[((t + 1) & 1) * 1152 + (quad * 4 + r) * 72 + 16 * w + l16] = (f16)(oo * reluf(c1[r]));
+          af1[kf] = *(const f16x8*)&h1db[(t & 1) * 1152 + l16 * 72 + kf * 32 + quad * 8];
+        f32x4 z[4];
+#pragma unroll
+        for (int gm = 0; gm < 4; gm++) {
+          f32x4 zz = {0.f, 0.f, 0.f, 0.f};
+#pragma unroll
+          for (int kf = 0; kf < 4; kf++)
+            zz = MFMA16(af0[kf], wrA[gm][kf], zz);
+#pragma unroll
+          for (int kf = 0; kf < 2; kf++)
+            zz = MFMA16(af1[kf], wrB[gm][kf], zz);
+          z[gm] = zz;
+        }
+#pragma unroll
+        for (int r = 0; r < 4; r++) {
+          float gi = sigm(z[0][r] + bt[0]);
+          float ff = sigm(z[1][r] + bt[1]);
+          float gg = reluf(z[2][r] + bt[2]);
+          float oo = sigm(z[3][r] + bt[3]);
+          c1[r] = ff * c1[r] + gi * gg;
+          h1db[((t + 1) & 1) * 1152 + (quad * 4 + r) * 72 + 16 * w16 + l16] =
+              (f16)(oo * reluf(c1[r]));
+        }
       }
     }
     __syncthreads();
@@ -612,24 +544,22 @@
     float* zmB = (float*)(smem + 8448);
     const f16* hf = h1db;
 #pragma unroll 1
-    for (int e = 0; e < 8; e++) {
-      const int idx = tid + 256 * e, sq = idx >> 7, j = idx & 127;
+    for (int e = 0; e < 2; e++) {
+      const int idx = tid + 1024 * e, sq = idx >> 7, j = idx & 127;
       float a = A.td0b[j];
       for (int k = 0; k < 64; k++) a += (float)hf[sq * 72 + k] * A.td0W[k * 128 + j];
       zmA[sq * 132 + j] = reluf(a);
     }
     __syncthreads();
-#pragma unroll 1
-    for (int e = 0; e < 4; e++) {
-      const int idx = tid + 256 * e, sq = idx >> 6, j = idx & 63;
+    {
+      const int sq = tid >> 6, j = tid & 63;
       float a = A.td1b[j];
       for (int k = 0; k < 128; k++) a += zmA[sq * 132 + k] * A.td1W[k * 64 + j];
       zmB[sq * 68 + j] = reluf(a);
     }
     __syncthreads();
-#pragma unroll 1
-    for (int e = 0; e < 2; e++) {
-      const int idx = tid + 256 * e, sq = idx >> 5, j = idx & 31;
+    if (tid < 512) {
+      const int sq = tid >> 5, j = tid & 31;
       float a = A.td2b[j];
       for (int k = 0; k < 64; k++) a += zmB[sq * 68 + k] * A.td2W[k * 32 + j];
       A.feat[(g * 16 + sq) * 64 + j] = a;
@@ -780,7 +710,7 @@
   ra.td2W = td2_W; ra.td2b = td2_b;
   ra.h0r = h0r; ra.h1r = h1r; ra.h0tr = h0tr; ra.cnt = cnt;
   ra.feat = feat;
-  recur_pipe<<<96, 256, 0, stream>>>(ra);
+  recur_pipe<<<40, 1024, 0, stream>>>(ra);
 
   head_kernel<<<1, 256, 0, stream>>>(feat, L0_W, L0_b, L1_W, L1_b, L2_W, L2_b,
                                      L3_W, L3_b, (float*)d_out);
```
